# Kernel optimization log

Measured on AMD Instinct MI355X. Metric: run time of the kernel, lower is better.

The kernel has to match this reference:

```python
import jax, jax.numpy as jnp
import numpy as np

TREE = 128
BASIC = 128
EPS = 1e-5


def layer_norm(x, g, b):
    m = jnp.mean(x, axis=-1, keepdims=True)
    v = jnp.mean((x - m) ** 2, axis=-1, keepdims=True)
    return (x - m) * jax.lax.rsqrt(v + EPS) * g + b


def setup_inputs() -> dict:
    key = jax.random.key(0)
    ks = jax.random.split(key, 32)
    n2, n1, n0 = 320000, 80000, 20000
    inp = {
        'subtree_h_top': jax.random.normal(ks[0], (n2, TREE), jnp.float32),
        'atom_x_1': jax.random.normal(ks[1], (n1, BASIC), jnp.float32),
        'atom_x_0': jax.random.normal(ks[2], (n0, BASIC), jnp.float32),
        'bond_x_2': jax.random.normal(ks[3], (n2, BASIC), jnp.float32),
        'bond_x_1': jax.random.normal(ks[4], (n1, BASIC), jnp.float32),
        'branch_W1': jax.random.normal(ks[5], (2, TREE + BASIC, TREE), jnp.float32) * 0.05,
        'branch_b1': jnp.zeros((2, TREE), jnp.float32),
        'branch_g1': jnp.ones((2, TREE), jnp.float32),
        'branch_beta1': jnp.zeros((2, TREE), jnp.float32),
        'branch_W2': jax.random.normal(ks[6], (2, TREE, TREE), jnp.float32) * 0.05,
        'branch_b2': jnp.zeros((2, TREE), jnp.float32),
        'branch_g2': jnp.ones((2, TREE), jnp.float32),
        'branch_beta2': jnp.zeros((2, TREE), jnp.float32),
        'sub_W1': jax.random.normal(ks[7], (2, BASIC + TREE, TREE), jnp.float32) * 0.05,
        'sub_b1': jnp.zeros((2, TREE), jnp.float32),
        'sub_g1': jnp.ones((2, TREE), jnp.float32),
        'sub_beta1': jnp.zeros((2, TREE), jnp.float32),
        'sub_W2': jax.random.normal(ks[8], (2, TREE, TREE), jnp.float32) * 0.05,
        'sub_b2': jnp.zeros((2, TREE), jnp.float32),
        'sub_g2': jnp.ones((2, TREE), jnp.float32),
        'sub_beta2': jnp.zeros((2, TREE), jnp.float32),
        'head_W': jax.random.normal(ks[9], (2, BASIC + TREE, TREE), jnp.float32) * 0.05,
        'head_b': jnp.zeros((2, TREE), jnp.float32),
        'head_g': jnp.ones((2, TREE), jnp.float32),
        'head_beta': jnp.zeros((2, TREE), jnp.float32),
        'src_2': jax.random.randint(ks[10], (n2,), 0, n2),
        'dst_2': jax.random.randint(ks[11], (n2,), 0, n1),
        'src_1': jax.random.randint(ks[12], (n1,), 0, n1),
        'dst_1': jax.random.randint(ks[13], (n1,), 0, n0),
    }
    return inp


def reference(subtree_h_top, atom_x_1, atom_x_0, bond_x_2, bond_x_1,
              branch_W1, branch_b1, branch_g1, branch_beta1,
              branch_W2, branch_b2, branch_g2, branch_beta2,
              sub_W1, sub_b1, sub_g1, sub_beta1,
              sub_W2, sub_b2, sub_g2, sub_beta2,
              head_W, head_b, head_g, head_beta,
              src_2, dst_2, src_1, dst_1):
    relu = jax.nn.relu
    h = subtree_h_top  # subtree_h of level tree_level nodes
    atom_xs = (atom_x_1, atom_x_0)
    bond_xs = (bond_x_2, bond_x_1)
    srcs = (src_2, src_1)
    dsts = (dst_2, dst_1)
    for i in range(2):  # i=0 -> k=2, i=1 -> k=1 (fixed small loop over tree levels)
        ax = atom_xs[i]
        # Branch_Update: edge MLP on [subtree_h[src], bond_x]
        ex = jnp.concatenate([h[srcs[i]], bond_xs[i]], axis=-1)  # [E, tree+basic]
        bh = relu(layer_norm(ex @ branch_W1[i] + branch_b1[i], branch_g1[i], branch_beta1[i]))
        bh = relu(layer_norm(bh @ branch_W2[i] + branch_b2[i], branch_g2[i], branch_beta2[i]))
        # fn.sum aggregation per destination (head) node
        agg = jax.ops.segment_sum(bh, dsts[i], num_segments=ax.shape[0])
        # Tree_Update_Sep
        sx = jnp.concatenate([ax, agg], axis=-1)  # [N, basic+tree]
        f = relu(layer_norm(sx @ sub_W1[i] + sub_b1[i], sub_g1[i], sub_beta1[i]))
        f = relu(layer_norm(f @ sub_W2[i] + sub_b2[i], sub_g2[i], sub_beta2[i]))
        th = jnp.concatenate([ax, f], axis=-1)
        h = relu(layer_norm(th @ head_W[i] + head_b[i], head_g[i], head_beta[i]))
    return h  # subtree_h of atom_0 nodes: [n0, tree_dim]
```

## Files before the change

kernel.cpp:

```cpp
#include <hip/hip_runtime.h>


#define D   128
#define TE  32
#define XS  264

typedef float  f32x4 __attribute__((ext_vector_type(4)));
typedef _Float16 f16x8 __attribute__((ext_vector_type(8)));

__device__ __forceinline__ unsigned short f2h(float f) {
    union { _Float16 h; unsigned short u; } x;
    x.h = (_Float16)f;
    return x.u;
}

__global__ __launch_bounds__(256) void pack_w(
    const float* __restrict__ brW1, const float* __restrict__ brW2,
    const float* __restrict__ sW1,  const float* __restrict__ sW2,
    const float* __restrict__ hW,   unsigned short* __restrict__ Wp)
{
    int p = blockIdx.x * 256 + threadIdx.x;
    const float* src; int off, K;
    if (p < 65536)       { src = brW1; off = 0;      K = 256; }
    else if (p < 98304)  { src = brW2; off = 65536;  K = 128; }
    else if (p < 163840) { src = sW1;  off = 98304;  K = 256; }
    else if (p < 196608) { src = sW2;  off = 163840; K = 128; }
    else                 { src = hW;   off = 196608; K = 256; }
    int q = p - off, lvl, r;
    if (K == 256) { lvl = q >> 15; r = q & 32767; }
    else          { lvl = q >> 14; r = q & 16383; }
    int kb = r >> 12, n = (r >> 5) & 127, kk = r & 31;
    Wp[p] = f2h(src[(size_t)lvl * K * 128 + (size_t)(kb * 32 + kk) * 128 + n]);
}


__global__ __launch_bounds__(256) void csr_hist(
    const int* __restrict__ dA, int EA, const int* __restrict__ dB, int EB,
    int* __restrict__ cnt, int AOFFv)
{
    int i = blockIdx.x * 256 + threadIdx.x;
    if (i < EA)               atomicAdd(cnt + dA[i], 1);
    else if (i - EA < EB)     atomicAdd(cnt + AOFFv + dB[i - EA], 1);
}

__global__ __launch_bounds__(256) void csr_scanA(
    const int* __restrict__ cnt, int* __restrict__ inc, int* __restrict__ bsum,
    int nbA, int AOFFv)
{
    __shared__ int lds[256];
    int b = blockIdx.x, t = threadIdx.x;
    int lb, ebase, bs;
    if (b < nbA) { lb = b;       ebase = 0;     bs = lb; }
    else         { lb = b - nbA; ebase = AOFFv; bs = 128 + lb; }
    int idx = ebase + lb * 1024 + t * 4;
    int s0 = cnt[idx], s1 = cnt[idx + 1], s2 = cnt[idx + 2], s3 = cnt[idx + 3];
    int p1 = s0 + s1, p2 = p1 + s2, p3 = p2 + s3;
    lds[t] = p3; __syncthreads();
#pragma unroll
    for (int o = 1; o < 256; o <<= 1) {
        int v = (t >= o) ? lds[t - o] : 0;
        __syncthreads();
        lds[t] += v;
        __syncthreads();
    }
    int ex = lds[t] - p3;
    inc[idx] = ex + s0; inc[idx + 1] = ex + p1; inc[idx + 2] = ex + p2; inc[idx + 3] = ex + p3;
    if (t == 255) bsum[bs] = lds[255];
}

__global__ __launch_bounds__(256) void csr_scanB(int* __restrict__ bsum, int nbA, int nbB)
{
    __shared__ int lds[256];
    int t = threadIdx.x, seg = t >> 7, i = t & 127;
    int n = seg ? nbB : nbA;
    lds[t] = (i < n) ? bsum[t] : 0;
    __syncthreads();
#pragma unroll
    for (int o = 1; o < 128; o <<= 1) {
        int v = (i >= o) ? lds[t - o] : 0;
        __syncthreads();
        lds[t] += v;
        __syncthreads();
    }
    if (i < n) bsum[t] = lds[t];
}

__global__ __launch_bounds__(256) void csr_scanC(
    const int* __restrict__ cnt, int* __restrict__ inc, const int* __restrict__ bsum,
    int* __restrict__ cursor, int nbA, int AOFFv)
{
    int b = blockIdx.x, t = threadIdx.x;
    int lb, ebase, bs;
    if (b < nbA) { lb = b;       ebase = 0;     bs = lb; }
    else         { lb = b - nbA; ebase = AOFFv; bs = 128 + lb; }
    int carry = (lb > 0) ? bsum[bs - 1] : 0;
    int idx = ebase + lb * 1024 + t * 4;
#pragma unroll
    for (int j = 0; j < 4; ++j) {
        int v = inc[idx + j] + carry;
        inc[idx + j] = v;
        cursor[idx + j] = v - cnt[idx + j];
    }
}

__global__ __launch_bounds__(256) void csr_pos(
    const int* __restrict__ dA, int EA, const int* __restrict__ dB, int EB,
    int* __restrict__ cursor, int* __restrict__ posA, int* __restrict__ posB, int AOFFv)
{
    int i = blockIdx.x * 256 + threadIdx.x;
    if (i < EA)           posA[i] = atomicAdd(cursor + dA[i], 1);
    else if (i - EA < EB) posB[i - EA] = atomicAdd(cursor + AOFFv + dB[i - EA], 1);
}


template<int KB>
__device__ __forceinline__ void gemm_f16(const unsigned short* s_in, int stride,
    const unsigned short* __restrict__ Wp, int rb, int cb, int n15, int q, f32x4 acc[4])
{
    f32x4 zero = {0.f, 0.f, 0.f, 0.f};
#pragma unroll
    for (int ct = 0; ct < 4; ++ct) acc[ct] = zero;
#pragma unroll
    for (int kb = 0; kb < KB; ++kb) {
        f16x8 af = *(const f16x8*)(s_in + (rb + n15) * stride + kb * 32 + q * 8);
        const unsigned short* wb = Wp + (size_t)kb * 4096 + q * 8;
#pragma unroll
        for (int ct = 0; ct < 4; ++ct) {
            f16x8 bf = *(const f16x8*)(wb + (cb + ct * 16 + n15) * 32);
            acc[ct] = __builtin_amdgcn_mfma_f32_16x16x32_f16(af, bf, acc[ct], 0, 0, 0);
        }
    }
}

__device__ __forceinline__ void ln_relu(f32x4 acc[4],
    const float* __restrict__ b, const float* __restrict__ g, const float* __restrict__ be,
    float* s_red, float* s_ms, int rb, int cb, int n15, int q, int wcol, int t)
{
#pragma unroll
    for (int ct = 0; ct < 4; ++ct) {
        float bb = b[cb + ct * 16 + n15];
#pragma unroll
        for (int r = 0; r < 4; ++r) acc[ct][r] += bb;
    }
    float sum[4], ss[4];
#pragma unroll
    for (int r = 0; r < 4; ++r) {
        sum[r] = acc[0][r] + acc[1][r] + acc[2][r] + acc[3][r];
        ss[r]  = acc[0][r]*acc[0][r] + acc[1][r]*acc[1][r]
               + acc[2][r]*acc[2][r] + acc[3][r]*acc[3][r];
    }
#pragma unroll
    for (int off = 1; off < 16; off <<= 1) {
#pragma unroll
        for (int r = 0; r < 4; ++r) {
            sum[r] += __shfl_xor(sum[r], off, 64);
            ss[r]  += __shfl_xor(ss[r],  off, 64);
        }
    }
    if (n15 == 0) {
#pragma unroll
        for (int r = 0; r < 4; ++r) {
            int row = rb + q * 4 + r;
            s_red[row * 4 + wcol * 2 + 0] = sum[r];
            s_red[row * 4 + wcol * 2 + 1] = ss[r];
        }
    }
    __syncthreads();
    if (t < TE) {
        float sm = s_red[t * 4 + 0] + s_red[t * 4 + 2];
        float sq = s_red[t * 4 + 1] + s_red[t * 4 + 3];
        float mean = sm * (1.f / 128.f);
        float var  = sq * (1.f / 128.f) - mean * mean;
        s_ms[t * 2 + 0] = mean;
        s_ms[t * 2 + 1] = rsqrtf(var + 1e-5f);
    }
    __syncthreads();
#pragma unroll
    for (int ct = 0; ct < 4; ++ct) {
        float gg = g[cb + ct * 16 + n15], bb = be[cb + ct * 16 + n15];
#pragma unroll
        for (int r = 0; r < 4; ++r) {
            int row = rb + q * 4 + r;
            float v = (acc[ct][r] - s_ms[row * 2 + 0]) * s_ms[row * 2 + 1] * gg + bb;
            acc[ct][r] = fmaxf(v, 0.f);
        }
    }
}

template<bool HBF16, bool CSR>
__global__ __launch_bounds__(256, 8) void edge_mlp(
    const void* __restrict__ hsrc, const float* __restrict__ bond,
    const int* __restrict__ src, const int* __restrict__ dstpos,
    const unsigned short* __restrict__ Wp1, const unsigned short* __restrict__ Wp2,
    const float* __restrict__ b1, const float* __restrict__ g1, const float* __restrict__ be1,
    const float* __restrict__ b2, const float* __restrict__ g2, const float* __restrict__ be2,
    float* __restrict__ agg, unsigned short* __restrict__ ebh, int E)
{
    __shared__ unsigned short s_x[TE * XS];
    __shared__ float s_red[TE * 4];
    __shared__ float s_ms[TE * 2];
    __shared__ int s_src[TE], s_idx[TE];
    unsigned short* s_y = s_x + 128;

    int t = threadIdx.x, eb = blockIdx.x * TE;
    if (t < TE) {
        int ge = eb + t;
        s_src[t] = (ge < E) ? src[ge] : -1;
        s_idx[t] = (ge < E) ? dstpos[ge] : -1;
    }
    __syncthreads();

    if (HBF16) {
        const unsigned short* hp = (const unsigned short*)hsrc;
        for (int c = t; c < TE * 16; c += 256) {
            int row = c >> 4, k8 = c & 15;
            int s = s_src[row];
            uint4 v = make_uint4(0, 0, 0, 0);
            if (s >= 0) v = *(const uint4*)(hp + (size_t)s * 128 + k8 * 8);
            *(uint4*)(s_x + row * XS + k8 * 8) = v;
        }
    } else {
        const float* hp = (const float*)hsrc;
        for (int c = t; c < TE * 32; c += 256) {
            int row = c >> 5, k4 = c & 31;
            int s = s_src[row];
            float4 v = make_float4(0, 0, 0, 0);
            if (s >= 0) v = *(const float4*)(hp + (size_t)s * 128 + k4 * 4);
            ushort4 o; o.x = f2h(v.x); o.y = f2h(v.y); o.z = f2h(v.z); o.w = f2h(v.w);
            *(ushort4*)(s_x + row * XS + k4 * 4) = o;
        }
    }
    for (int c = t; c < TE * 32; c += 256) {
        int row = c >> 5, k4 = c & 31;
        int ge = eb + row;
        float4 v = make_float4(0, 0, 0, 0);
        if (ge < E) v = *(const float4*)(bond + (size_t)ge * 128 + k4 * 4);
        ushort4 o; o.x = f2h(v.x); o.y = f2h(v.y); o.z = f2h(v.z); o.w = f2h(v.w);
        *(ushort4*)(s_x + row * XS + 128 + k4 * 4) = o;
    }
    __syncthreads();

    int l = t & 63, w = t >> 6;
    int n15 = l & 15, q = l >> 4;
    int rb = (w & 1) * 16, cb = (w >> 1) * 64, wcol = w >> 1;

    f32x4 acc[4];
    gemm_f16<8>(s_x, XS, Wp1, rb, cb, n15, q, acc);
    ln_relu(acc, b1, g1, be1, s_red, s_ms, rb, cb, n15, q, wcol, t);
#pragma unroll
    for (int ct = 0; ct < 4; ++ct)
#pragma unroll
        for (int r = 0; r < 4; ++r)
            s_y[(rb + q * 4 + r) * XS + cb + ct * 16 + n15] = f2h(acc[ct][r]);
    __syncthreads();
    gemm_f16<4>(s_y, XS, Wp2, rb, cb, n15, q, acc);
    ln_relu(acc, b2, g2, be2, s_red, s_ms, rb, cb, n15, q, wcol, t);

    if (CSR) {
#pragma unroll
        for (int ct = 0; ct < 4; ++ct)
#pragma unroll
            for (int r = 0; r < 4; ++r)
                s_x[(rb + q * 4 + r) * XS + cb + ct * 16 + n15] = f2h(acc[ct][r]);
        __syncthreads();
        for (int c = t; c < TE * 16; c += 256) {
            int row = c >> 4, k8 = c & 15;
            int p = s_idx[row];
            if (p >= 0)
                *(uint4*)(ebh + (size_t)p * 128 + k8 * 8) =
                    *(const uint4*)(s_x + row * XS + k8 * 8);
        }
    } else {
#pragma unroll
        for (int ct = 0; ct < 4; ++ct)
#pragma unroll
            for (int r = 0; r < 4; ++r) {
                int row = rb + q * 4 + r;
                int gd = s_idx[row];
                if (gd >= 0)
                    atomicAdd(agg + (size_t)gd * D + cb + ct * 16 + n15, acc[ct][r]);
            }
    }
}

template<bool OUT_F16, bool CSR>
__global__ __launch_bounds__(256, 8) void node_mlp(
    const float* __restrict__ ax, const float* __restrict__ agg,
    const int* __restrict__ inc, const unsigned short* __restrict__ ebh,
    const unsigned short* __restrict__ Wp1, const unsigned short* __restrict__ Wp2,
    const unsigned short* __restrict__ Wp3,
    const float* __restrict__ b1, const float* __restrict__ g1, const float* __restrict__ be1,
    const float* __restrict__ b2, const float* __restrict__ g2, const float* __restrict__ be2,
    const float* __restrict__ b3, const float* __restrict__ g3, const float* __restrict__ be3,
    void* __restrict__ out, int N)
{
    __shared__ unsigned short s_x[TE * XS];
    __shared__ float s_red[TE * 4];
    __shared__ float s_ms[TE * 2];
    __shared__ int s_beg[TE], s_end[TE];
    unsigned short* s_y = s_x + 128;

    int t = threadIdx.x, nb = blockIdx.x * TE;

    if (CSR && t < TE) {
        int gr = nb + t, b0 = 0, e0 = 0;
        if (gr < N) { e0 = inc[gr]; b0 = (gr == 0) ? 0 : inc[gr - 1]; }
        s_beg[t] = b0; s_end[t] = e0;
    }

    for (int c = t; c < TE * 32; c += 256) {
        int row = c >> 5, k4 = c & 31;
        int gr = nb + row;
        float4 v = make_float4(0, 0, 0, 0);
        if (gr < N) v = *(const float4*)(ax + (size_t)gr * 128 + k4 * 4);
        ushort4 o; o.x = f2h(v.x); o.y = f2h(v.y); o.z = f2h(v.z); o.w = f2h(v.w);
        *(ushort4*)(s_x + row * XS + k4 * 4) = o;
    }

    if (CSR) {
        __syncthreads();
        int r = t >> 3, s8 = t & 7;
        float a[16];
#pragma unroll
        for (int k = 0; k < 16; ++k) a[k] = 0.f;
        int jb = s_beg[r], je = s_end[r];
        for (int j = jb; j < je; ++j) {
            const unsigned short* rp = ebh + (size_t)j * 128 + s8 * 16;
            f16x8 v0 = *(const f16x8*)rp;
            f16x8 v1 = *(const f16x8*)(rp + 8);
#pragma unroll
            for (int k = 0; k < 8; ++k) { a[k] += (float)v0[k]; a[8 + k] += (float)v1[k]; }
        }
        f16x8 h0, h1;
#pragma unroll
        for (int k = 0; k < 8; ++k) { h0[k] = (_Float16)a[k]; h1[k] = (_Float16)a[8 + k]; }
        unsigned short* op = s_x + r * XS + 128 + s8 * 16;
        *(f16x8*)op = h0;
        *(f16x8*)(op + 8) = h1;
    } else {
        for (int c = t; c < TE * 32; c += 256) {
            int row = c >> 5, k4 = c & 31;
            int gr = nb + row;
            float4 v = make_float4(0, 0, 0, 0);
            if (gr < N) v = *(const float4*)(agg + (size_t)gr * 128 + k4 * 4);
            ushort4 o; o.x = f2h(v.x); o.y = f2h(v.y); o.z = f2h(v.z); o.w = f2h(v.w);
            *(ushort4*)(s_x + row * XS + 128 + k4 * 4) = o;
        }
    }
    __syncthreads();

    int l = t & 63, w = t >> 6;
    int n15 = l & 15, q = l >> 4;
    int rb = (w & 1) * 16, cb = (w >> 1) * 64, wcol = w >> 1;

    f32x4 acc[4];
    gemm_f16<8>(s_x, XS, Wp1, rb, cb, n15, q, acc);
    ln_relu(acc, b1, g1, be1, s_red, s_ms, rb, cb, n15, q, wcol, t);
#pragma unroll
    for (int ct = 0; ct < 4; ++ct)
#pragma unroll
        for (int r = 0; r < 4; ++r)
            s_y[(rb + q * 4 + r) * XS + cb + ct * 16 + n15] = f2h(acc[ct][r]);
    __syncthreads();
    gemm_f16<4>(s_y, XS, Wp2, rb, cb, n15, q, acc);
    ln_relu(acc, b2, g2, be2, s_red, s_ms, rb, cb, n15, q, wcol, t);
#pragma unroll
    for (int ct = 0; ct < 4; ++ct)
#pragma unroll
        for (int r = 0; r < 4; ++r)
            s_x[(rb + q * 4 + r) * XS + 128 + cb + ct * 16 + n15] = f2h(acc[ct][r]);
    __syncthreads();
    gemm_f16<8>(s_x, XS, Wp3, rb, cb, n15, q, acc);
    ln_relu(acc, b3, g3, be3, s_red, s_ms, rb, cb, n15, q, wcol, t);

#pragma unroll
    for (int ct = 0; ct < 4; ++ct)
#pragma unroll
        for (int r = 0; r < 4; ++r) {
            int row = rb + q * 4 + r;
            int gr = nb + row;
            int col = cb + ct * 16 + n15;
            if (gr < N) {
                if (OUT_F16)
                    ((unsigned short*)out)[(size_t)gr * D + col] = f2h(acc[ct][r]);
                else
                    ((float*)out)[(size_t)gr * D + col] = acc[ct][r];
            }
        }
}

extern "C" void kernel_launch(void* const* d_in, const int* in_sizes, int n_in,
                              void* d_out, int out_size, void* d_ws, size_t ws_size,
                              hipStream_t stream)
{
    const float* h2   = (const float*)d_in[0];
    const float* ax1  = (const float*)d_in[1];
    const float* ax0  = (const float*)d_in[2];
    const float* bx2  = (const float*)d_in[3];
    const float* bx1  = (const float*)d_in[4];
    const float* brW1 = (const float*)d_in[5];
    const float* brb1 = (const float*)d_in[6];
    const float* brg1 = (const float*)d_in[7];
    const float* brbe1= (const float*)d_in[8];
    const float* brW2 = (const float*)d_in[9];
    const float* brb2 = (const float*)d_in[10];
    const float* brg2 = (const float*)d_in[11];
    const float* brbe2= (const float*)d_in[12];
    const float* sW1  = (const float*)d_in[13];
    const float* sb1  = (const float*)d_in[14];
    const float* sg1  = (const float*)d_in[15];
    const float* sbe1 = (const float*)d_in[16];
    const float* sW2  = (const float*)d_in[17];
    const float* sb2  = (const float*)d_in[18];
    const float* sg2  = (const float*)d_in[19];
    const float* sbe2 = (const float*)d_in[20];
    const float* hW   = (const float*)d_in[21];
    const float* hb   = (const float*)d_in[22];
    const float* hg   = (const float*)d_in[23];
    const float* hbe  = (const float*)d_in[24];
    const int*   src2 = (const int*)d_in[25];
    const int*   dst2 = (const int*)d_in[26];
    const int*   src1 = (const int*)d_in[27];
    const int*   dst1 = (const int*)d_in[28];

    int n2 = in_sizes[0] / D;
    int n1 = in_sizes[1] / D;
    int n0 = in_sizes[2] / D;

    unsigned short* Wp = (unsigned short*)d_ws;

    const unsigned short* pBr1[2] = { Wp + 0,      Wp + 32768 };
    const unsigned short* pBr2[2] = { Wp + 65536,  Wp + 65536  + 16384 };
    const unsigned short* pS1 [2] = { Wp + 98304,  Wp + 98304  + 32768 };
    const unsigned short* pS2 [2] = { Wp + 163840, Wp + 163840 + 16384 };
    const unsigned short* pH  [2] = { Wp + 196608, Wp + 196608 + 32768 };

    int nbA = (n1 + 1023) / 1024, nbB = (n0 + 1023) / 1024;
    int AOFFv = nbA * 1024;
    size_t AN = (size_t)AOFFv + (size_t)nbB * 1024;
    auto al = [](size_t x) { return (x + 255) & ~(size_t)255; };
    size_t o = 524288;
    size_t cnt_o  = o; o = al(o + AN * 4);
    size_t inc_o  = o; o = al(o + AN * 4);
    size_t cur_o  = o; o = al(o + AN * 4);
    size_t bsum_o = o; o = al(o + 1024);
    size_t posA_o = o; o = al(o + (size_t)n2 * 4);
    size_t posB_o = o; o = al(o + (size_t)n1 * 4);
    size_t h1_o   = o; o = al(o + (size_t)n1 * 256);
    size_t ebh_o  = o; o = al(o + (size_t)n2 * 256);
    bool use_csr = (ws_size >= o) && (nbA <= 128) && (nbB <= 128);

    pack_w<<<dim3(1024), dim3(256), 0, stream>>>(brW1, brW2, sW1, sW2, hW, Wp);

    if (use_csr) {
        int*            cnt    = (int*)((char*)d_ws + cnt_o);
        int*            inc    = (int*)((char*)d_ws + inc_o);
        int*            cursor = (int*)((char*)d_ws + cur_o);
        int*            bsum   = (int*)((char*)d_ws + bsum_o);
        int*            posA   = (int*)((char*)d_ws + posA_o);
        int*            posB   = (int*)((char*)d_ws + posB_o);
        unsigned short* h1     = (unsigned short*)((char*)d_ws + h1_o);
        unsigned short* ebh    = (unsigned short*)((char*)d_ws + ebh_o);

        int EG = (n2 + n1 + 255) / 256;
        hipMemsetAsync(cnt, 0, AN * 4, stream);
        csr_hist <<<dim3(EG),        dim3(256), 0, stream>>>(dst2, n2, dst1, n1, cnt, AOFFv);
        csr_scanA<<<dim3(nbA + nbB), dim3(256), 0, stream>>>(cnt, inc, bsum, nbA, AOFFv);
        csr_scanB<<<dim3(1),         dim3(256), 0, stream>>>(bsum, nbA, nbB);
        csr_scanC<<<dim3(nbA + nbB), dim3(256), 0, stream>>>(cnt, inc, bsum, cursor, nbA, AOFFv);
        csr_pos  <<<dim3(EG),        dim3(256), 0, stream>>>(dst2, n2, dst1, n1, cursor, posA, posB, AOFFv);

        edge_mlp<false, true><<<dim3((n2 + TE - 1) / TE), dim3(256), 0, stream>>>(
            h2, bx2, src2, posA, pBr1[0], pBr2[0],
            brb1, brg1, brbe1, brb2, brg2, brbe2, nullptr, ebh, n2);
        node_mlp<true, true><<<dim3((n1 + TE - 1) / TE), dim3(256), 0, stream>>>(
            ax1, nullptr, inc, ebh, pS1[0], pS2[0], pH[0],
            sb1, sg1, sbe1, sb2, sg2, sbe2, hb, hg, hbe, h1, n1);

        edge_mlp<true, true><<<dim3((n1 + TE - 1) / TE), dim3(256), 0, stream>>>(
            h1, bx1, src1, posB, pBr1[1], pBr2[1],
            brb1 + D, brg1 + D, brbe1 + D, brb2 + D, brg2 + D, brbe2 + D, nullptr, ebh, n1);
        node_mlp<false, true><<<dim3((n0 + TE - 1) / TE), dim3(256), 0, stream>>>(
            ax0, nullptr, inc + AOFFv, ebh, pS1[1], pS2[1], pH[1],
            sb1 + D, sg1 + D, sbe1 + D, sb2 + D, sg2 + D, sbe2 + D,
            hb + D, hg + D, hbe + D, d_out, n0);
    } else {
        float*          agg = (float*)((char*)d_ws + 524288);
        unsigned short* h1  = (unsigned short*)(agg + (size_t)n1 * D);

        hipMemsetAsync(agg, 0, (size_t)n1 * D * sizeof(float), stream);
        edge_mlp<false, false><<<dim3((n2 + TE - 1) / TE), dim3(256), 0, stream>>>(
            h2, bx2, src2, dst2, pBr1[0], pBr2[0],
            brb1, brg1, brbe1, brb2, brg2, brbe2, agg, nullptr, n2);
        node_mlp<true, false><<<dim3((n1 + TE - 1) / TE), dim3(256), 0, stream>>>(
            ax1, agg, nullptr, nullptr, pS1[0], pS2[0], pH[0],
            sb1, sg1, sbe1, sb2, sg2, sbe2, hb, hg, hbe, h1, n1);

        hipMemsetAsync(agg, 0, (size_t)n0 * D * sizeof(float), stream);
        edge_mlp<true, false><<<dim3((n1 + TE - 1) / TE), dim3(256), 0, stream>>>(
            h1, bx1, src1, dst1, pBr1[1], pBr2[1],
            brb1 + D, brg1 + D, brbe1 + D, brb2 + D, brg2 + D, brbe2 + D, agg, nullptr, n1);
        node_mlp<false, false><<<dim3((n0 + TE - 1) / TE), dim3(256), 0, stream>>>(
            ax0, agg, nullptr, nullptr, pS1[1], pS2[1], pH[1],
            sb1 + D, sg1 + D, sbe1 + D, sb2 + D, sg2 + D, sbe2 + D,
            hb + D, hg + D, hbe + D, d_out, n0);
    }
}
```

Before: 715.7 us.

## Double the row tile to 64 so each wave reuses weight fragments across two M tiles

The per-block row tile grows from 32 to 64, and each wave now computes two 16-row MFMA tiles that share the same weight fragment load. This halves weight-fragment global/L2 traffic per row and the number of blocks. The CSR aggregation loop is remapped to 4 threads per row with 32 columns each, and launch bounds drop to 4 blocks per SM. In exchange, LDS use per block doubles, register pressure rises and occupancy falls.

```diff
diff --git a/kernel.cpp b/kernel.cpp
--- a/kernel.cpp
+++ b/kernel.cpp
@@ -2,7 +2,7 @@
 
 
 #define D   128
-#define TE  32
+#define TE  64
 #define XS  264
 
 typedef float  f32x4 __attribute__((ext_vector_type(4)));
@@ -115,24 +115,28 @@
 
 template<int KB>
 __device__ __forceinline__ void gemm_f16(const unsigned short* s_in, int stride,
-    const unsigned short* __restrict__ Wp, int rb, int cb, int n15, int q, f32x4 acc[4])
+    const unsigned short* __restrict__ Wp, int rb, int cb, int n15, int q, f32x4 acc[2][4])
 {
     f32x4 zero = {0.f, 0.f, 0.f, 0.f};
 #pragma unroll
-    for (int ct = 0; ct < 4; ++ct) acc[ct] = zero;
+    for (int m = 0; m < 2; ++m)
+#pragma unroll
+        for (int ct = 0; ct < 4; ++ct) acc[m][ct] = zero;
 #pragma unroll
     for (int kb = 0; kb < KB; ++kb) {
-        f16x8 af = *(const f16x8*)(s_in + (rb + n15) * stride + kb * 32 + q * 8);
+        f16x8 af0 = *(const f16x8*)(s_in + (rb + n15) * stride + kb * 32 + q * 8);
+        f16x8 af1 = *(const f16x8*)(s_in + (rb + 16 + n15) * stride + kb * 32 + q * 8);
         const unsigned short* wb = Wp + (size_t)kb * 4096 + q * 8;
 #pragma unroll
         for (int ct = 0; ct < 4; ++ct) {
             f16x8 bf = *(const f16x8*)(wb + (cb + ct * 16 + n15) * 32);
-            acc[ct] = __builtin_amdgcn_mfma_f32_16x16x32_f16(af, bf, acc[ct], 0, 0, 0);
-        }
-    }
-}
-
-__device__ __forceinline__ void ln_relu(f32x4 acc[4],
+            acc[0][ct] = __builtin_amdgcn_mfma_f32_16x16x32_f16(af0, bf, acc[0][ct], 0, 0, 0);
+            acc[1][ct] = __builtin_amdgcn_mfma_f32_16x16x32_f16(af1, bf, acc[1][ct], 0, 0, 0);
+        }
+    }
+}
+
+__device__ __forceinline__ void ln_relu(f32x4 acc[2][4],
     const float* __restrict__ b, const float* __restrict__ g, const float* __restrict__ be,
     float* s_red, float* s_ms, int rb, int cb, int n15, int q, int wcol, int t)
 {
@@ -140,30 +144,38 @@
     for (int ct = 0; ct < 4; ++ct) {
         float bb = b[cb + ct * 16 + n15];
 #pragma unroll
-        for (int r = 0; r < 4; ++r) acc[ct][r] += bb;
-    }
-    float sum[4], ss[4];
-#pragma unroll
-    for (int r = 0; r < 4; ++r) {
-        sum[r] = acc[0][r] + acc[1][r] + acc[2][r] + acc[3][r];
-        ss[r]  = acc[0][r]*acc[0][r] + acc[1][r]*acc[1][r]
-               + acc[2][r]*acc[2][r] + acc[3][r]*acc[3][r];
-    }
+        for (int m = 0; m < 2; ++m)
+#pragma unroll
+            for (int r = 0; r < 4; ++r) acc[m][ct][r] += bb;
+    }
+    float sum[2][4], ss[2][4];
+#pragma unroll
+    for (int m = 0; m < 2; ++m)
+#pragma unroll
+        for (int r = 0; r < 4; ++r) {
+            sum[m][r] = acc[m][0][r] + acc[m][1][r] + acc[m][2][r] + acc[m][3][r];
+            ss[m][r]  = acc[m][0][r]*acc[m][0][r] + acc[m][1][r]*acc[m][1][r]
+                      + acc[m][2][r]*acc[m][2][r] + acc[m][3][r]*acc[m][3][r];
+        }
 #pragma unroll
     for (int off = 1; off < 16; off <<= 1) {
 #pragma unroll
-        for (int r = 0; r < 4; ++r) {
-            sum[r] += __shfl_xor(sum[r], off, 64);
-            ss[r]  += __shfl_xor(ss[r],  off, 64);
-        }
+        for (int m = 0; m < 2; ++m)
+#pragma unroll
+            for (int r = 0; r < 4; ++r) {
+                sum[m][r] += __shfl_xor(sum[m][r], off, 64);
+                ss[m][r]  += __shfl_xor(ss[m][r],  off, 64);
+            }
     }
     if (n15 == 0) {
 #pragma unroll
-        for (int r = 0; r < 4; ++r) {
-            int row = rb + q * 4 + r;
-            s_red[row * 4 + wcol * 2 + 0] = sum[r];
-            s_red[row * 4 + wcol * 2 + 1] = ss[r];
-        }
+        for (int m = 0; m < 2; ++m)
+#pragma unroll
+            for (int r = 0; r < 4; ++r) {
+                int row = rb + m * 16 + q * 4 + r;
+                s_red[row * 4 + wcol * 2 + 0] = sum[m][r];
+                s_red[row * 4 + wcol * 2 + 1] = ss[m][r];
+            }
     }
     __syncthreads();
     if (t < TE) {
@@ -179,16 +191,18 @@
     for (int ct = 0; ct < 4; ++ct) {
         float gg = g[cb + ct * 16 + n15], bb = be[cb + ct * 16 + n15];
 #pragma unroll
-        for (int r = 0; r < 4; ++r) {
-            int row = rb + q * 4 + r;
-            float v = (acc[ct][r] - s_ms[row * 2 + 0]) * s_ms[row * 2 + 1] * gg + bb;
-            acc[ct][r] = fmaxf(v, 0.f);
-        }
+        for (int m = 0; m < 2; ++m)
+#pragma unroll
+            for (int r = 0; r < 4; ++r) {
+                int row = rb + m * 16 + q * 4 + r;
+                float v = (acc[m][ct][r] - s_ms[row * 2 + 0]) * s_ms[row * 2 + 1] * gg + bb;
+                acc[m][ct][r] = fmaxf(v, 0.f);
+            }
     }
 }
 
 template<bool HBF16, bool CSR>
-__global__ __launch_bounds__(256, 8) void edge_mlp(
+__global__ __launch_bounds__(256, 4) void edge_mlp(
     const void* __restrict__ hsrc, const float* __restrict__ bond,
     const int* __restrict__ src, const int* __restrict__ dstpos,
     const unsigned short* __restrict__ Wp1, const unsigned short* __restrict__ Wp2,
@@ -242,26 +256,30 @@
 
     int l = t & 63, w = t >> 6;
     int n15 = l & 15, q = l >> 4;
-    int rb = (w & 1) * 16, cb = (w >> 1) * 64, wcol = w >> 1;
-
-    f32x4 acc[4];
+    int rb = (w & 1) * 32, cb = (w >> 1) * 64, wcol = w >> 1;
+
+    f32x4 acc[2][4];
     gemm_f16<8>(s_x, XS, Wp1, rb, cb, n15, q, acc);
     ln_relu(acc, b1, g1, be1, s_red, s_ms, rb, cb, n15, q, wcol, t);
 #pragma unroll
-    for (int ct = 0; ct < 4; ++ct)
-#pragma unroll
-        for (int r = 0; r < 4; ++r)
-            s_y[(rb + q * 4 + r) * XS + cb + ct * 16 + n15] = f2h(acc[ct][r]);
+    for (int m = 0; m < 2; ++m)
+#pragma unroll
+        for (int ct = 0; ct < 4; ++ct)
+#pragma unroll
+            for (int r = 0; r < 4; ++r)
+                s_y[(rb + m * 16 + q * 4 + r) * XS + cb + ct * 16 + n15] = f2h(acc[m][ct][r]);
     __syncthreads();
     gemm_f16<4>(s_y, XS, Wp2, rb, cb, n15, q, acc);
     ln_relu(acc, b2, g2, be2, s_red, s_ms, rb, cb, n15, q, wcol, t);
 
     if (CSR) {
 #pragma unroll
-        for (int ct = 0; ct < 4; ++ct)
-#pragma unroll
-            for (int r = 0; r < 4; ++r)
-                s_x[(rb + q * 4 + r) * XS + cb + ct * 16 + n15] = f2h(acc[ct][r]);
+        for (int m = 0; m < 2; ++m)
+#pragma unroll
+            for (int ct = 0; ct < 4; ++ct)
+#pragma unroll
+                for (int r = 0; r < 4; ++r)
+                    s_x[(rb + m * 16 + q * 4 + r) * XS + cb + ct * 16 + n15] = f2h(acc[m][ct][r]);
         __syncthreads();
         for (int c = t; c < TE * 16; c += 256) {
             int row = c >> 4, k8 = c & 15;
@@ -272,19 +290,21 @@
         }
     } else {
 #pragma unroll
-        for (int ct = 0; ct < 4; ++ct)
-#pragma unroll
-            for (int r = 0; r < 4; ++r) {
-                int row = rb + q * 4 + r;
-                int gd = s_idx[row];
-                if (gd >= 0)
-                    atomicAdd(agg + (size_t)gd * D + cb + ct * 16 + n15, acc[ct][r]);
-            }
+        for (int m = 0; m < 2; ++m)
+#pragma unroll
+            for (int ct = 0; ct < 4; ++ct)
+#pragma unroll
+                for (int r = 0; r < 4; ++r) {
+                    int row = rb + m * 16 + q * 4 + r;
+                    int gd = s_idx[row];
+                    if (gd >= 0)
+                        atomicAdd(agg + (size_t)gd * D + cb + ct * 16 + n15, acc[m][ct][r]);
+                }
     }
 }
 
 template<bool OUT_F16, bool CSR>
-__global__ __launch_bounds__(256, 8) void node_mlp(
+__global__ __launch_bounds__(256, 4) void node_mlp(
     const float* __restrict__ ax, const float* __restrict__ agg,
     const int* __restrict__ inc, const unsigned short* __restrict__ ebh,
     const unsigned short* __restrict__ Wp1, const unsigned short* __restrict__ Wp2,
@@ -319,24 +339,33 @@
 
     if (CSR) {
         __syncthreads();
-        int r = t >> 3, s8 = t & 7;
-        float a[16];
-#pragma unroll
-        for (int k = 0; k < 16; ++k) a[k] = 0.f;
+        int r = t >> 2, s4 = t & 3;
+        float a[32];
+#pragma unroll
+        for (int k = 0; k < 32; ++k) a[k] = 0.f;
         int jb = s_beg[r], je = s_end[r];
         for (int j = jb; j < je; ++j) {
-            const unsigned short* rp = ebh + (size_t)j * 128 + s8 * 16;
+            const unsigned short* rp = ebh + (size_t)j * 128 + s4 * 32;
             f16x8 v0 = *(const f16x8*)rp;
             f16x8 v1 = *(const f16x8*)(rp + 8);
-#pragma unroll
-            for (int k = 0; k < 8; ++k) { a[k] += (float)v0[k]; a[8 + k] += (float)v1[k]; }
-        }
-        f16x8 h0, h1;
-#pragma unroll
-        for (int k = 0; k < 8; ++k) { h0[k] = (_Float16)a[k]; h1[k] = (_Float16)a[8 + k]; }
-        unsigned short* op = s_x + r * XS + 128 + s8 * 16;
-        *(f16x8*)op = h0;
-        *(f16x8*)(op + 8) = h1;
+            f16x8 v2 = *(const f16x8*)(rp + 16);
+            f16x8 v3 = *(const f16x8*)(rp + 24);
+#pragma unroll
+            for (int k = 0; k < 8; ++k) {
+                a[k]      += (float)v0[k];
+                a[8 + k]  += (float)v1[k];
+                a[16 + k] += (float)v2[k];
+                a[24 + k] += (float)v3[k];
+            }
+        }
+        unsigned short* op = s_x + r * XS + 128 + s4 * 32;
+#pragma unroll
+        for (int blk = 0; blk < 4; ++blk) {
+            f16x8 h;
+#pragma unroll
+            for (int k = 0; k < 8; ++k) h[k] = (_Float16)a[blk * 8 + k];
+            *(f16x8*)(op + blk * 8) = h;
+        }
     } else {
         for (int c = t; c < TE * 32; c += 256) {
             int row = c >> 5, k4 = c & 31;
@@ -351,42 +380,48 @@
 
     int l = t & 63, w = t >> 6;
     int n15 = l & 15, q = l >> 4;
-    int rb = (w & 1) * 16, cb = (w >> 1) * 64, wcol = w >> 1;
-
-    f32x4 acc[4];
+    int rb = (w & 1) * 32, cb = (w >> 1) * 64, wcol = w >> 1;
+
+    f32x4 acc[2][4];
     gemm_f16<8>(s_x, XS, Wp1, rb, cb, n15, q, acc);
     ln_relu(acc, b1, g1, be1, s_red, s_ms, rb, cb, n15, q, wcol, t);
 #pragma unroll
-    for (int ct = 0; ct < 4; ++ct)
-#pragma unroll
-        for (int r = 0; r < 4; ++r)
-            s_y[(rb + q * 4 + r) * XS + cb + ct * 16 + n15] = f2h(acc[ct][r]);
+    for (int m = 0; m < 2; ++m)
+#pragma unroll
+        for (int ct = 0; ct < 4; ++ct)
+#pragma unroll
+            for (int r = 0; r < 4; ++r)
+                s_y[(rb + m * 16 + q * 4 + r) * XS + cb + ct * 16 + n15] = f2h(acc[m][ct][r]);
     __syncthreads();
     gemm_f16<4>(s_y, XS, Wp2, rb, cb, n15, q, acc);
     ln_relu(acc, b2, g2, be2, s_red, s_ms, rb, cb, n15, q, wcol, t);
 #pragma unroll
-    for (int ct = 0; ct < 4; ++ct)
-#pragma unroll
-        for (int r = 0; r < 4; ++r)
-            s_x[(rb + q * 4 + r) * XS + 128 + cb + ct * 16 + n15] = f2h(acc[ct][r]);
+    for (int m = 0; m < 2; ++m)
+#pragma unroll
+        for (int ct = 0; ct < 4; ++ct)
+#pragma unroll
+            for (int r = 0; r < 4; ++r)
+                s_x[(rb + m * 16 + q * 4 + r) * XS + 128 + cb + ct * 16 + n15] = f2h(acc[m][ct][r]);
     __syncthreads();
     gemm_f16<8>(s_x, XS, Wp3, rb, cb, n15, q, acc);
     ln_relu(acc, b3, g3, be3, s_red, s_ms, rb, cb, n15, q, wcol, t);
 
 #pragma unroll
-    for (int ct = 0; ct < 4; ++ct)
-#pragma unroll
-        for (int r = 0; r < 4; ++r) {
-            int row = rb + q * 4 + r;
-            int gr = nb + row;
-            int col = cb + ct * 16 + n15;
-            if (gr < N) {
-                if (OUT_F16)
-                    ((unsigned short*)out)[(size_t)gr * D + col] = f2h(acc[ct][r]);
-                else
-                    ((float*)out)[(size_t)gr * D + col] = acc[ct][r];
+    for (int m = 0; m < 2; ++m)
+#pragma unroll
+        for (int ct = 0; ct < 4; ++ct)
+#pragma unroll
+            for (int r = 0; r < 4; ++r) {
+                int row = rb + m * 16 + q * 4 + r;
+                int gr = nb + row;
+                int col = cb + ct * 16 + n15;
+                if (gr < N) {
+                    if (OUT_F16)
+                        ((unsigned short*)out)[(size_t)gr * D + col] = f2h(acc[m][ct][r]);
+                    else
+                        ((float*)out)[(size_t)gr * D + col] = acc[m][ct][r];
+                }
             }
-        }
 }
 
 extern "C" void kernel_launch(void* const* d_in, const int* in_sizes, int n_in,
```

Measured after the change: 682.6 us. -4.6%, faster.
